# Optimization experiments

Hardware: AMD Instinct MI355X
Metric: run time of the kernel (lower is better)

The kernel has to match this reference:

```python
import jax, jax.numpy as jnp
import numpy as np

N_NODES = 100000
N_EDGES = 3200000
N_FEAT = 64
N_CLASS = 16


def setup_inputs() -> dict:
    key = jax.random.key(0)
    k1, k2, k3, k4 = jax.random.split(key, 4)
    x = jax.random.normal(k1, (N_NODES, N_FEAT), dtype=jnp.float32)
    weight = jax.random.normal(k2, (N_CLASS, N_FEAT), dtype=jnp.float32) * 0.1
    bias = jax.random.normal(k3, (N_CLASS,), dtype=jnp.float32) * 0.1
    edge_index = jax.random.randint(k4, (2, N_EDGES), 0, N_NODES, dtype=jnp.int64)
    return {"x": x, "weight": weight, "bias": bias, "edge_index": edge_index, "k": 3}


def reference(x, weight, bias, edge_index, k):
    # SGConv: x' = (D^-1/2 (A + I) D^-1/2)^K X, then Linear, then log_softmax.
    n = x.shape[0]
    loop = jnp.arange(n, dtype=edge_index.dtype)
    src = jnp.concatenate([edge_index[0], loop])  # add self-loops
    dst = jnp.concatenate([edge_index[1], loop])
    # gcn_norm: degree over destination nodes (edge weights all ones)
    deg = jax.ops.segment_sum(jnp.ones_like(src, dtype=x.dtype), dst, num_segments=n)
    dis = jnp.where(deg > 0, jax.lax.rsqrt(jnp.maximum(deg, 1)), 0.0).astype(x.dtype)
    norm = dis[src] * dis[dst]  # [E + N]
    for _ in range(k):
        # gather source features, scale, scatter-add to destinations
        x = jax.ops.segment_sum(x[src] * norm[:, None], dst, num_segments=n)
    logits = x @ weight.T + bias  # [N, C]
    return jax.nn.log_softmax(logits, axis=1)
```

## Files before the change

kernel.cpp:

```cpp
#include <hip/hip_runtime.h>
#include <hip/hip_fp16.h>

#define NFEAT 64
#define NCLS 16
#define MAXDEG 96
#define BSH 7
#define BSIZE 128
#define NBLK 512
#define NBMAX 1024
#define EPB 6272
#define CAP 4480
#define MINCP 32

__global__ void k_binsort(const int* __restrict__ src, const int* __restrict__ dst,
                          int* __restrict__ gcnt, int* __restrict__ pairs,
                          int nE, int epb, int nb) {
    __shared__ int ebuf[EPB];
    __shared__ int gbuf[EPB];
    __shared__ int cnt[NBMAX];
    __shared__ int gb[NBMAX];
    __shared__ int wt[NBMAX / 64];
    int j = blockIdx.x, tid = threadIdx.x;
    int lane = tid & 63, wv = tid >> 6;
    cnt[tid] = 0;
    __syncthreads();
    int e0 = j * epb, e1 = min(e0 + epb, nE);
    for (int e = e0 + tid; e < e1; e += blockDim.x)
        atomicAdd(&cnt[dst[e] >> BSH], 1);
    __syncthreads();
    int v = cnt[tid];
    int s = v;
#pragma unroll
    for (int off = 1; off < 64; off <<= 1) {
        int u = __shfl_up(s, off);
        if (lane >= off) s += u;
    }
    if (lane == 63) wt[wv] = s;
    __syncthreads();
    int pre = 0;
#pragma unroll
    for (int w = 0; w < NBMAX / 64; ++w) if (w < wv) pre += wt[w];
    int excl = pre + s - v;
    cnt[tid] = excl;
    if (tid < nb) {
        int g = tid * CAP;
        if (v > 0) g += atomicAdd(&gcnt[tid], v);
        gb[tid] = g - excl;
    }
    __syncthreads();
    for (int e = e0 + tid; e < e1; e += blockDim.x) {
        int d = dst[e], ssrc = src[e];
        int b = d >> BSH;
        int p = atomicAdd(&cnt[b], 1);
        ebuf[p] = ((d & (BSIZE - 1)) << 17) | ssrc;
        gbuf[p] = gb[b] + p;
    }
    __syncthreads();
    int m = e1 - e0;
    for (int p = tid; p < m; p += blockDim.x)
        pairs[gbuf[p]] = ebuf[p];
}

__global__ void k_csr(const int* __restrict__ pairs, const int* __restrict__ btot,
                      int* __restrict__ ssortP, int4* __restrict__ aux,
                      float* __restrict__ dis, int n, int nb) {
    __shared__ int buf[BSIZE][MAXDEG];
    __shared__ int cnt[BSIZE];
    int b = blockIdx.x;
    for (int t = threadIdx.x; t < BSIZE; t += blockDim.x) cnt[t] = 0;
    __syncthreads();
    int e0 = b * CAP, e1 = e0 + btot[b];
    for (int e = e0 + threadIdx.x; e < e1; e += blockDim.x) {
        int pk = pairs[e];
        int s = pk & 0x1FFFF;
        int ld = ((unsigned)pk) >> 17;
        int p = atomicAdd(&cnt[ld], 1);
        if (p < MAXDEG) buf[ld][p] = s;
    }
    __syncthreads();
    for (int idx = threadIdx.x; idx < BSIZE * MAXDEG; idx += blockDim.x) {
        int ld = idx / MAXDEG, p = idx - ld * MAXDEG;
        int node = (b << BSH) + ld;
        int c = min(cnt[ld], MAXDEG - 1);
        int cp = (c + 1 + 15) & ~15;
        if (cp < MINCP) cp = MINCP;
        if (node < n && p < cp) {
            int val = (p < c) ? buf[ld][p] : ((p == c) ? node : n);
            ssortP[(size_t)node * MAXDEG + p] = val;
        }
    }
    int node = (b << BSH) + threadIdx.x;
    if (threadIdx.x < BSIZE && node < n) {
        int c = min(cnt[threadIdx.x], MAXDEG - 1);
        float d = (float)(c + 1);
        float ds = rsqrtf(d);
        dis[node] = ds;
        aux[node] = make_int4(c + 1, __float_as_int(ds * ds), __float_as_int(sqrtf(d)), 0);
    }
}

__global__ void k_lin0(const float* __restrict__ x, const float* __restrict__ w,
                       const float* __restrict__ dis, __half* __restrict__ za,
                       __half* __restrict__ zb, int n) {
    __shared__ float4 ws4[NCLS * 17];
    for (int i = threadIdx.x; i < NCLS * 16; i += blockDim.x) {
        int c = i >> 4, j = i & 15;
        ws4[c * 17 + j] = ((const float4*)w)[i];
    }
    __syncthreads();
    int t = blockIdx.x * blockDim.x + threadIdx.x;
    int node = t >> 2;
    if (node > n) return;
    int q = t & 3;
    if (node == n) {
        ((int2*)(za + (size_t)n * NCLS))[q] = make_int2(0, 0);
        ((int2*)(zb + (size_t)n * NCLS))[q] = make_int2(0, 0);
        return;
    }
    const float4* xr = (const float4*)(x + (size_t)node * NFEAT);
    const float4* wq = &ws4[(q << 2) * 17];
    float a0 = 0.f, a1 = 0.f, a2 = 0.f, a3 = 0.f;
#pragma unroll
    for (int j = 0; j < 16; ++j) {
        float4 v  = xr[j];
        float4 w0 = wq[j];
        float4 w1 = wq[17 + j];
        float4 w2 = wq[34 + j];
        float4 w3 = wq[51 + j];
        a0 += v.x * w0.x + v.y * w0.y + v.z * w0.z + v.w * w0.w;
        a1 += v.x * w1.x + v.y * w1.y + v.z * w1.z + v.w * w1.w;
        a2 += v.x * w2.x + v.y * w2.y + v.z * w2.z + v.w * w2.w;
        a3 += v.x * w3.x + v.y * w3.y + v.z * w3.z + v.w * w3.w;
    }
    float d = dis[node];
    __half2 h01 = __floats2half2_rn(a0 * d, a1 * d);
    __half2 h23 = __floats2half2_rn(a2 * d, a3 * d);
    __half2* o = (__half2*)(za + (size_t)node * NCLS) + (q << 1);
    o[0] = h01;
    o[1] = h23;
}

__device__ inline void acc8(int4 v, float* a) {
    __half2 t; float2 f;
    *(int*)&t = v.x; f = __half22float2(t); a[0] += f.x; a[1] += f.y;
    *(int*)&t = v.y; f = __half22float2(t); a[2] += f.x; a[3] += f.y;
    *(int*)&t = v.z; f = __half22float2(t); a[4] += f.x; a[5] += f.y;
    *(int*)&t = v.w; f = __half22float2(t); a[6] += f.x; a[7] += f.y;
}
__device__ inline int pkh2(float x, float y) {
    __half2 r = __floats2half2_rn(x, y);
    return *(int*)&r;
}

template <bool FINAL>
__global__ void __launch_bounds__(256, 8)
k_prop16(const __half* __restrict__ zin, __half* __restrict__ zout,
         const int4* __restrict__ aux, const int* __restrict__ ssortP,
         const float* __restrict__ bias, float* __restrict__ out, int n) {
    int t = blockIdx.x * blockDim.x + threadIdx.x;
    int wid = t >> 6;
    int lane = threadIdx.x & 63;
    int g2 = lane >> 4;
    int e3 = (lane >> 1) & 7;
    int h8 = (lane & 1) << 3;
    int node = wid * 4 + g2;
    bool valid = node < n;
    int nd = valid ? node : (n - 1);
    int4 ax = aux[nd];
    const int* row = ssortP + (size_t)nd * MAXDEG + 2 * e3;
    int2 r0 = *(const int2*)(row);
    int2 r1 = *(const int2*)(row + 16);
    int dg = ax.x;
    if (dg > MAXDEG) dg = MAXDEG;
    int2 r2 = make_int2(n, n), r3 = r2, r4 = r2, r5 = r2;
    if (dg > 32) r2 = *(const int2*)(row + 32);
    if (dg > 48) r3 = *(const int2*)(row + 48);
    if (dg > 64) r4 = *(const int2*)(row + 64);
    if (dg > 80) r5 = *(const int2*)(row + 80);
    float a[8] = {0.f, 0.f, 0.f, 0.f, 0.f, 0.f, 0.f, 0.f};
#define GATH2(rr) { \
        int4 vA = *(const int4*)(zin + (size_t)(rr).x * NCLS + h8); \
        int4 vB = *(const int4*)(zin + (size_t)(rr).y * NCLS + h8); \
        acc8(vA, a); acc8(vB, a); }
    GATH2(r0);
    GATH2(r1);
    if (dg > 32) GATH2(r2);
    if (dg > 48) GATH2(r3);
    if (dg > 64) GATH2(r4);
    if (dg > 80) GATH2(r5);
#undef GATH2
#pragma unroll
    for (int i = 0; i < 8; ++i) {
        a[i] += __shfl_xor(a[i], 2);
        a[i] += __shfl_xor(a[i], 4);
        a[i] += __shfl_xor(a[i], 8);
    }
    float d2 = __int_as_float(ax.y);
    if (!FINAL) {
        if (valid && e3 == 0) {
            int4 o = make_int4(pkh2(a[0] * d2, a[1] * d2), pkh2(a[2] * d2, a[3] * d2),
                               pkh2(a[4] * d2, a[5] * d2), pkh2(a[6] * d2, a[7] * d2));
            *(int4*)(zout + (size_t)node * NCLS + h8) = o;
        }
    } else {
        float rd = __int_as_float(ax.z);
        float sc = d2 * rd;
        int hq = h8 >> 2;
        float4 b0 = ((const float4*)bias)[hq];
        float4 b1 = ((const float4*)bias)[hq + 1];
        float lg[8];
        lg[0] = a[0] * sc + b0.x; lg[1] = a[1] * sc + b0.y;
        lg[2] = a[2] * sc + b0.z; lg[3] = a[3] * sc + b0.w;
        lg[4] = a[4] * sc + b1.x; lg[5] = a[5] * sc + b1.y;
        lg[6] = a[6] * sc + b1.z; lg[7] = a[7] * sc + b1.w;
        float m = fmaxf(fmaxf(fmaxf(lg[0], lg[1]), fmaxf(lg[2], lg[3])),
                        fmaxf(fmaxf(lg[4], lg[5]), fmaxf(lg[6], lg[7])));
        m = fmaxf(m, __shfl_xor(m, 1));
        float s = 0.f;
#pragma unroll
        for (int i = 0; i < 8; ++i) s += expf(lg[i] - m);
        s += __shfl_xor(s, 1);
        float lse = m + logf(s);
        if (valid && e3 == 0) {
            float* orow = out + (size_t)node * NCLS + h8;
            ((float4*)orow)[0] = make_float4(lg[0] - lse, lg[1] - lse, lg[2] - lse, lg[3] - lse);
            ((float4*)orow)[1] = make_float4(lg[4] - lse, lg[5] - lse, lg[6] - lse, lg[7] - lse);
        }
    }
}

extern "C" void kernel_launch(void* const* d_in, const int* in_sizes, int n_in,
                              void* d_out, int out_size, void* d_ws, size_t ws_size,
                              hipStream_t stream) {
    const float* x    = (const float*)d_in[0];
    const float* w    = (const float*)d_in[1];
    const float* bias = (const float*)d_in[2];
    const int*   ei   = (const int*)d_in[3];

    int n  = in_sizes[0] / NFEAT;
    int nE = in_sizes[3] / 2;
    const int* src = ei;
    const int* dst = ei + nE;

    int nb  = (n + BSIZE - 1) >> BSH;
    int epb = (nE + NBLK - 1) / NBLK;

    char* p = (char*)d_ws;
    auto alloc = [&](size_t bytes) { void* r = (void*)p; p += (bytes + 511) & ~511ULL; return r; };
    int*    ssortP = (int*)alloc((size_t)n * MAXDEG * 4);
    int*    pairs  = (int*)alloc((size_t)nb * CAP * 4);
    __half* za     = (__half*)alloc((size_t)(n + 1) * NCLS * 2);
    __half* zb     = (__half*)alloc((size_t)(n + 1) * NCLS * 2);
    int4*   aux    = (int4*)alloc((size_t)n * 16);
    float*  dis    = (float*)alloc((size_t)n * 4);
    int*    gcnt   = (int*)alloc((size_t)nb * 4);

    hipMemsetAsync(gcnt, 0, (size_t)nb * 4, stream);
    k_binsort<<<NBLK, 1024, 0, stream>>>(src, dst, gcnt, pairs, nE, epb, nb);
    k_csr    <<<nb, 512, 0, stream>>>(pairs, gcnt, ssortP, aux, dis, n, nb);

    k_lin0<<<(4 * (n + 1) + 255) / 256, 256, 0, stream>>>(x, w, dis, za, zb, n);

    int nblk = (int)((((size_t)(n + 3) / 4) * 64 + 255) / 256);
    k_prop16<false><<<nblk, 256, 0, stream>>>(za, zb, aux, ssortP, bias, nullptr, n);
    k_prop16<false><<<nblk, 256, 0, stream>>>(zb, za, aux, ssortP, bias, nullptr, n);
    k_prop16<true> <<<nblk, 256, 0, stream>>>(za, nullptr, aux, ssortP, bias, (float*)d_out, n);
}
```

Before: 132.0 us.

## Replace two-pass bin sort CSR build with direct global-atomic scatter

Removes the shared-memory bin sort and the per-bin CSR kernel. Each edge now claims a slot with a global atomicAdd on a per-node counter and writes its source index straight into the padded ELL-style neighbour table. Padding, the self-loop slot and the degree and normalisation values are filled inside the first linear kernel, which saves one launch and the intermediate pairs buffer. The cost is 3.2M global atomics on random addresses plus scattered 4-byte stores, and neighbour order within a row is no longer deterministic.

```diff
diff --git a/kernel.cpp b/kernel.cpp
--- a/kernel.cpp
+++ b/kernel.cpp
@@ -4,103 +4,37 @@
 #define NFEAT 64
 #define NCLS 16
 #define MAXDEG 96
-#define BSH 7
-#define BSIZE 128
-#define NBLK 512
-#define NBMAX 1024
-#define EPB 6272
-#define CAP 4480
 #define MINCP 32
 
-__global__ void k_binsort(const int* __restrict__ src, const int* __restrict__ dst,
-                          int* __restrict__ gcnt, int* __restrict__ pairs,
-                          int nE, int epb, int nb) {
-    __shared__ int ebuf[EPB];
-    __shared__ int gbuf[EPB];
-    __shared__ int cnt[NBMAX];
-    __shared__ int gb[NBMAX];
-    __shared__ int wt[NBMAX / 64];
-    int j = blockIdx.x, tid = threadIdx.x;
-    int lane = tid & 63, wv = tid >> 6;
-    cnt[tid] = 0;
-    __syncthreads();
-    int e0 = j * epb, e1 = min(e0 + epb, nE);
-    for (int e = e0 + tid; e < e1; e += blockDim.x)
-        atomicAdd(&cnt[dst[e] >> BSH], 1);
-    __syncthreads();
-    int v = cnt[tid];
-    int s = v;
-#pragma unroll
-    for (int off = 1; off < 64; off <<= 1) {
-        int u = __shfl_up(s, off);
-        if (lane >= off) s += u;
-    }
-    if (lane == 63) wt[wv] = s;
-    __syncthreads();
-    int pre = 0;
-#pragma unroll
-    for (int w = 0; w < NBMAX / 64; ++w) if (w < wv) pre += wt[w];
-    int excl = pre + s - v;
-    cnt[tid] = excl;
-    if (tid < nb) {
-        int g = tid * CAP;
-        if (v > 0) g += atomicAdd(&gcnt[tid], v);
-        gb[tid] = g - excl;
-    }
-    __syncthreads();
-    for (int e = e0 + tid; e < e1; e += blockDim.x) {
-        int d = dst[e], ssrc = src[e];
-        int b = d >> BSH;
-        int p = atomicAdd(&cnt[b], 1);
-        ebuf[p] = ((d & (BSIZE - 1)) << 17) | ssrc;
-        gbuf[p] = gb[b] + p;
-    }
-    __syncthreads();
-    int m = e1 - e0;
-    for (int p = tid; p < m; p += blockDim.x)
-        pairs[gbuf[p]] = ebuf[p];
-}
-
-__global__ void k_csr(const int* __restrict__ pairs, const int* __restrict__ btot,
-                      int* __restrict__ ssortP, int4* __restrict__ aux,
-                      float* __restrict__ dis, int n, int nb) {
-    __shared__ int buf[BSIZE][MAXDEG];
-    __shared__ int cnt[BSIZE];
-    int b = blockIdx.x;
-    for (int t = threadIdx.x; t < BSIZE; t += blockDim.x) cnt[t] = 0;
-    __syncthreads();
-    int e0 = b * CAP, e1 = e0 + btot[b];
-    for (int e = e0 + threadIdx.x; e < e1; e += blockDim.x) {
-        int pk = pairs[e];
-        int s = pk & 0x1FFFF;
-        int ld = ((unsigned)pk) >> 17;
-        int p = atomicAdd(&cnt[ld], 1);
-        if (p < MAXDEG) buf[ld][p] = s;
-    }
-    __syncthreads();
-    for (int idx = threadIdx.x; idx < BSIZE * MAXDEG; idx += blockDim.x) {
-        int ld = idx / MAXDEG, p = idx - ld * MAXDEG;
-        int node = (b << BSH) + ld;
-        int c = min(cnt[ld], MAXDEG - 1);
-        int cp = (c + 1 + 15) & ~15;
-        if (cp < MINCP) cp = MINCP;
-        if (node < n && p < cp) {
-            int val = (p < c) ? buf[ld][p] : ((p == c) ? node : n);
-            ssortP[(size_t)node * MAXDEG + p] = val;
+__global__ void __launch_bounds__(256) k_scatter(const int* __restrict__ src,
+                                                 const int* __restrict__ dst,
+                                                 int* __restrict__ cnt,
+                                                 int* __restrict__ ssortP, int nE) {
+    int t = blockIdx.x * blockDim.x + threadIdx.x;
+    int e = t * 4;
+    if (e + 4 <= nE) {
+        int4 d4 = *(const int4*)(dst + e);
+        int4 s4 = *(const int4*)(src + e);
+        int p0 = atomicAdd(&cnt[d4.x], 1);
+        int p1 = atomicAdd(&cnt[d4.y], 1);
+        int p2 = atomicAdd(&cnt[d4.z], 1);
+        int p3 = atomicAdd(&cnt[d4.w], 1);
+        if (p0 < MAXDEG - 1) ssortP[(size_t)d4.x * MAXDEG + p0] = s4.x;
+        if (p1 < MAXDEG - 1) ssortP[(size_t)d4.y * MAXDEG + p1] = s4.y;
+        if (p2 < MAXDEG - 1) ssortP[(size_t)d4.z * MAXDEG + p2] = s4.z;
+        if (p3 < MAXDEG - 1) ssortP[(size_t)d4.w * MAXDEG + p3] = s4.w;
+    } else {
+        for (; e < nE; ++e) {
+            int d = dst[e], s = src[e];
+            int p = atomicAdd(&cnt[d], 1);
+            if (p < MAXDEG - 1) ssortP[(size_t)d * MAXDEG + p] = s;
         }
     }
-    int node = (b << BSH) + threadIdx.x;
-    if (threadIdx.x < BSIZE && node < n) {
-        int c = min(cnt[threadIdx.x], MAXDEG - 1);
-        float d = (float)(c + 1);
-        float ds = rsqrtf(d);
-        dis[node] = ds;
-        aux[node] = make_int4(c + 1, __float_as_int(ds * ds), __float_as_int(sqrtf(d)), 0);
-    }
 }
 
 __global__ void k_lin0(const float* __restrict__ x, const float* __restrict__ w,
-                       const float* __restrict__ dis, __half* __restrict__ za,
+                       const int* __restrict__ cnt, int* __restrict__ ssortP,
+                       int4* __restrict__ aux, __half* __restrict__ za,
                        __half* __restrict__ zb, int n) {
     __shared__ float4 ws4[NCLS * 17];
     for (int i = threadIdx.x; i < NCLS * 16; i += blockDim.x) {
@@ -117,6 +51,15 @@
         ((int2*)(zb + (size_t)n * NCLS))[q] = make_int2(0, 0);
         return;
     }
+    int c = min(cnt[node], MAXDEG - 1);
+    int cp = (c + 1 + 15) & ~15;
+    if (cp < MINCP) cp = MINCP;
+    for (int p = c + q; p < cp; p += 4)
+        ssortP[(size_t)node * MAXDEG + p] = (p == c) ? node : n;
+    float dd = (float)(c + 1);
+    float ds = rsqrtf(dd);
+    if (q == 0)
+        aux[node] = make_int4(c + 1, __float_as_int(ds * ds), __float_as_int(sqrtf(dd)), 0);
     const float4* xr = (const float4*)(x + (size_t)node * NFEAT);
     const float4* wq = &ws4[(q << 2) * 17];
     float a0 = 0.f, a1 = 0.f, a2 = 0.f, a3 = 0.f;
@@ -132,9 +75,8 @@
         a2 += v.x * w2.x + v.y * w2.y + v.z * w2.z + v.w * w2.w;
         a3 += v.x * w3.x + v.y * w3.y + v.z * w3.z + v.w * w3.w;
     }
-    float d = dis[node];
-    __half2 h01 = __floats2half2_rn(a0 * d, a1 * d);
-    __half2 h23 = __floats2half2_rn(a2 * d, a3 * d);
+    __half2 h01 = __floats2half2_rn(a0 * ds, a1 * ds);
+    __half2 h23 = __floats2half2_rn(a2 * ds, a3 * ds);
     __half2* o = (__half2*)(za + (size_t)node * NCLS) + (q << 1);
     o[0] = h01;
     o[1] = h23;
@@ -242,24 +184,18 @@
     const int* src = ei;
     const int* dst = ei + nE;
 
-    int nb  = (n + BSIZE - 1) >> BSH;
-    int epb = (nE + NBLK - 1) / NBLK;
-
     char* p = (char*)d_ws;
     auto alloc = [&](size_t bytes) { void* r = (void*)p; p += (bytes + 511) & ~511ULL; return r; };
     int*    ssortP = (int*)alloc((size_t)n * MAXDEG * 4);
-    int*    pairs  = (int*)alloc((size_t)nb * CAP * 4);
     __half* za     = (__half*)alloc((size_t)(n + 1) * NCLS * 2);
     __half* zb     = (__half*)alloc((size_t)(n + 1) * NCLS * 2);
     int4*   aux    = (int4*)alloc((size_t)n * 16);
-    float*  dis    = (float*)alloc((size_t)n * 4);
-    int*    gcnt   = (int*)alloc((size_t)nb * 4);
-
-    hipMemsetAsync(gcnt, 0, (size_t)nb * 4, stream);
-    k_binsort<<<NBLK, 1024, 0, stream>>>(src, dst, gcnt, pairs, nE, epb, nb);
-    k_csr    <<<nb, 512, 0, stream>>>(pairs, gcnt, ssortP, aux, dis, n, nb);
-
-    k_lin0<<<(4 * (n + 1) + 255) / 256, 256, 0, stream>>>(x, w, dis, za, zb, n);
+    int*    cnt    = (int*)alloc((size_t)n * 4);
+
+    hipMemsetAsync(cnt, 0, (size_t)n * 4, stream);
+    int sblk = (nE / 4 + 255) / 256;
+    k_scatter<<<sblk, 256, 0, stream>>>(src, dst, cnt, ssortP, nE);
+    k_lin0<<<(4 * (n + 1) + 255) / 256, 256, 0, stream>>>(x, w, cnt, ssortP, aux, za, zb, n);
 
     int nblk = (int)((((size_t)(n + 3) / 4) * 64 + 255) / 256);
     k_prop16<false><<<nblk, 256, 0, stream>>>(za, zb, aux, ssortP, bias, nullptr, n);
```

Result: slower. 375.2 us (+184.2%).
